# Kernel optimization log

Measured on AMD Instinct MI355X. Metric: run time of the kernel, lower is better.

The kernel has to match this reference:

```python
import jax, jax.numpy as jnp
import numpy as np

THRESHOLD = 0.05
TOP_N = 300
NMS_THR = 0.6
POST_TOP_N = 100
MIN_SIZE = 0
N_CLASS = 81
C = N_CLASS - 1
STRIDES = (8, 16, 32, 64, 128)
IMG_H, IMG_W = 800, 1024
B = 16


def _level_hw(s):
    return (-(-IMG_H // s), -(-IMG_W // s))


def setup_inputs() -> dict:
    key = jax.random.key(0)
    inp = {}
    for li, s in enumerate(STRIDES):
        H, W = _level_hw(s)
        key, k1, k2, k3 = jax.random.split(key, 4)
        xs = (jnp.arange(W, dtype=jnp.float32) + 0.5) * s
        ys = (jnp.arange(H, dtype=jnp.float32) + 0.5) * s
        gx, gy = jnp.meshgrid(xs, ys)  # [H, W], row-major h*W+w flatten order
        inp[f"location{li}"] = jnp.stack([gx.reshape(-1), gy.reshape(-1)], -1)
        inp[f"cls{li}"] = jax.random.normal(k1, (B, C, H, W), jnp.float32)
        inp[f"box{li}"] = jax.random.uniform(k2, (B, 4, H, W), jnp.float32) * (4.0 * s)
        inp[f"ctr{li}"] = jax.random.normal(k3, (B, 1, H, W), jnp.float32)
    inp["img_h"] = IMG_H
    inp["img_w"] = IMG_W
    return inp


def _process_level(loc, cls, box, ctr, img_h, img_w):
    b, c, h, w = cls.shape
    cls = jax.nn.sigmoid(cls.transpose(0, 2, 3, 1).reshape(b, h * w, c))
    box = box.transpose(0, 2, 3, 1).reshape(b, h * w, 4)
    ctr = jax.nn.sigmoid(ctr.reshape(b, h * w))
    score = cls * ctr[:, :, None]                 # [B, HW, C]
    masked = jnp.where(cls > THRESHOLD, score, -1.0).reshape(b, -1)
    k = min(TOP_N, masked.shape[1])
    vals, idx = jax.lax.top_k(masked, k)
    if k < TOP_N:
        vals = jnp.pad(vals, ((0, 0), (0, TOP_N - k)), constant_values=-1.0)
        idx = jnp.pad(idx, ((0, 0), (0, TOP_N - k)))
    valid = vals > 0.0                            # candidates only; pads invalid
    pos = idx // c
    label = idx % c + 1
    ssel = jnp.take_along_axis(score.reshape(b, -1), idx, axis=1)  # differentiable gather
    bsel = jnp.take_along_axis(box, pos[..., None], axis=1)        # [B, TOP_N, 4]
    lsel = loc[pos]                                                # [B, TOP_N, 2]
    # decode + clip (BoxList.clip clamps to [0, size-1])
    x1 = jnp.clip(lsel[..., 0] - bsel[..., 0], 0.0, img_w - 1.0)
    y1 = jnp.clip(lsel[..., 1] - bsel[..., 1], 0.0, img_h - 1.0)
    x2 = jnp.clip(lsel[..., 0] + bsel[..., 2], 0.0, img_w - 1.0)
    y2 = jnp.clip(lsel[..., 1] + bsel[..., 3], 0.0, img_h - 1.0)
    det = jnp.stack([x1, y1, x2, y2], -1)
    # remove_small_box: xywh with remove=1
    valid = valid & ((x2 - x1 + 1.0) >= MIN_SIZE) & ((y2 - y1 + 1.0) >= MIN_SIZE)
    scores = jnp.sqrt(jnp.maximum(ssel, 1e-12))
    return det, scores, label, valid


def _pairwise_iou(b):
    area = (b[:, 2] - b[:, 0]) * (b[:, 3] - b[:, 1])
    lt = jnp.maximum(b[:, None, :2], b[None, :, :2])
    rb = jnp.minimum(b[:, None, 2:], b[None, :, 2:])
    wh = jnp.clip(rb - lt, 0.0)
    inter = wh[..., 0] * wh[..., 1]
    union = area[:, None] + area[None, :] - inter
    return inter / jnp.maximum(union, 1e-9)


def _nms_image(boxes, scores, labels, valid, offset):
    # per-class NMS via class-offset trick: boxes of different labels never overlap
    K = boxes.shape[0]
    s = jnp.where(valid, scores, -jnp.inf)
    order = jnp.argsort(-s)
    b = boxes[order]
    v = valid[order]
    lab = labels[order]
    so = s[order]
    iou = _pairwise_iou(b + (lab.astype(b.dtype) * offset)[:, None])
    ar = jnp.arange(K)

    def body(i, keep):
        sup = (iou[i] > NMS_THR) & keep[i] & (ar > i)
        return keep & ~sup

    keep = jax.lax.fori_loop(0, K, body, v)
    s2 = jnp.where(keep, so, -jnp.inf)
    _, idx2 = jax.lax.top_k(s2, POST_TOP_N)   # post_top_n selection
    fvalid = jnp.take(keep, idx2)
    fb = jnp.where(fvalid[:, None], b[idx2], 0.0)
    fs = jnp.where(fvalid, so[idx2], 0.0)
    fl = jnp.where(fvalid, lab[idx2], 0)
    return fb, fs, fl, fvalid


def _forward(locs, clss, boxs, ctrs, img_h, img_w):
    dets, scs, labs, vals = [], [], [], []
    for loc, cl, bx, ct in zip(locs, clss, boxs, ctrs):
        d, s, l, v = _process_level(loc, cl, bx, ct, float(img_h), float(img_w))
        dets.append(d); scs.append(s); labs.append(l); vals.append(v)
    det = jnp.concatenate(dets, 1)   # [B, 5*TOP_N, 4]
    sc = jnp.concatenate(scs, 1)
    lab = jnp.concatenate(labs, 1)
    val = jnp.concatenate(vals, 1)
    offset = float(max(img_h, img_w) + 1)
    fb, fs, fl, fv = jax.vmap(lambda b_, s_, l_, v_: _nms_image(b_, s_, l_, v_, offset))(det, sc, lab, val)
    out5 = jnp.concatenate([fb, fs[..., None]], -1)  # [B, POST_TOP_N, 5]
    return out5, fl, fv


def reference(location0, location1, location2, location3, location4,
              cls0, cls1, cls2, cls3, cls4,
              box0, box1, box2, box3, box4,
              ctr0, ctr1, ctr2, ctr3, ctr4,
              img_h, img_w):
    locs = [location0, location1, location2, location3, location4]
    clss = [cls0, cls1, cls2, cls3, cls4]
    boxs = [box0, box1, box2, box3, box4]
    ctrs = [ctr0, ctr1, ctr2, ctr3, ctr4]
    return _forward(locs, clss, boxs, ctrs, img_h, img_w)
```

## Files before the change

### kernel.cpp

```cpp
#include <hip/hip_runtime.h>
#include <math.h>

#define THREADS 256
#define SORTT 1024

constexpr int NLEV  = 5;
constexpr int NB    = 16;
constexpr int NC    = 80;
constexpr int TOPN  = 300;
constexpr int KC    = NLEV * TOPN;
constexpr int KROWS = 1536;
constexpr int WORDS = 24;
constexpr int POSTN = 100;
constexpr int CAP   = 4096;
constexpr int NBINS = 2048;
constexpr int NPAIR = NLEV * NB;

constexpr int HW0 = 12800, HW1 = 3200, HW2 = 800, HW3 = 208, HW4 = 56;
constexpr int CH0 = 63, CH1 = 16, CH2 = 4, CH3 = 2, CH4 = 1;
constexpr int CHUNKS = CH0 + CH1 + CH2 + CH3 + CH4;
constexpr int CHUNK_ELEMS = 16384;

constexpr int SCTB0 = 0;
constexpr int SCTB1 = 204800;
constexpr int SCTB2 = 256000;
constexpr int SCTB3 = 268800;
constexpr int SCTB4 = 272128;
constexpr int SCTN  = 273024;

constexpr int GPL0 = 4000, GPL1 = 1000, GPL2 = 250, GPL3 = 65, GPL4 = 18;
constexpr int GMXB0 = 0;
constexpr int GMXB1 = GMXB0 + NB * GPL0;
constexpr int GMXB2 = GMXB1 + NB * GPL1;
constexpr int GMXB3 = GMXB2 + NB * GPL2;
constexpr int GMXB4 = GMXB3 + NB * GPL3;
constexpr int GMXN  = GMXB4 + NB * GPL4;

constexpr size_t align256(size_t x) { return (x + 255) & ~(size_t)255; }
constexpr size_t OFF_HIST = 0;
constexpr size_t OFF_CNT  = OFF_HIST + (size_t)NPAIR * NBINS * 4;
constexpr size_t OFF_CAND = align256(OFF_CNT + (size_t)NPAIR * 4);
constexpr size_t OFF_CBOX = align256(OFF_CAND + (size_t)NPAIR * CAP * 8);
constexpr size_t OFF_CSC  = align256(OFF_CBOX + (size_t)NB * KC * 4 * 4);
constexpr size_t OFF_CLB  = align256(OFF_CSC  + (size_t)NB * KC * 4);
constexpr size_t OFF_SSC  = align256(OFF_CLB  + (size_t)NB * KC * 4);
constexpr size_t OFF_SLB  = align256(OFF_SSC  + (size_t)NB * KC * 4);
constexpr size_t OFF_SBOX = align256(OFF_SLB  + (size_t)NB * KC * 4);
constexpr size_t OFF_OBOX = align256(OFF_SBOX + (size_t)NB * KC * 4 * 4);
constexpr size_t OFF_M    = align256(OFF_OBOX + (size_t)NB * KC * 4 * 4);
constexpr size_t OFF_SCT  = align256(OFF_M + (size_t)NB * KROWS * WORDS * 8);
constexpr size_t OFF_GMX  = align256(OFF_SCT + (size_t)SCTN * 4);
constexpr size_t OFF_TV   = align256(OFF_GMX + (size_t)GMXN * 2);

struct Cand { float s; int i; };

__device__ __forceinline__ float sigm(float x) { return 1.0f / (1.0f + expf(-x)); }

__device__ __forceinline__ float sigf(float x) {
#if __has_builtin(__builtin_amdgcn_exp2f) && __has_builtin(__builtin_amdgcn_rcpf)
    float e = __builtin_amdgcn_exp2f(__fmul_rn(x, -1.44269504088896340736f));
    return __builtin_amdgcn_rcpf(__fadd_rn(1.0f, e));
#else
    return 1.0f / (1.0f + __expf(-x));
#endif
}

__device__ __forceinline__ unsigned scoreKey(float s) {
    unsigned b = __float_as_uint(s);
    unsigned k = (b < 0x3E800000u) ? 0u : ((b - 0x3E800000u) >> 13);
    return (k > 2047u) ? 2047u : k;
}

__device__ __forceinline__ unsigned long long readlane64(unsigned long long v, int l) {
    unsigned lo = (unsigned)__builtin_amdgcn_readlane((int)(unsigned)(v & 0xffffffffull), l);
    unsigned hi = (unsigned)__builtin_amdgcn_readlane((int)(unsigned)(v >> 32), l);
    return ((unsigned long long)hi << 32) | lo;
}

__device__ void bitonicShared(float* ss, int* si, int N) {
    for (int k = 2; k <= N; k <<= 1) {
        for (int j = k >> 1; j > 0; j >>= 1) {
            __syncthreads();
            for (int i = threadIdx.x; i < N; i += blockDim.x) {
                int ixj = i ^ j;
                if (ixj > i) {
                    float s1 = ss[i], s2 = ss[ixj];
                    int a1 = si[i], a2 = si[ixj];
                    bool bef = (s1 > s2) || (s1 == s2 && a1 < a2);
                    bool up = ((i & k) == 0);
                    if (up ? !bef : bef) { ss[i] = s2; ss[ixj] = s1; si[i] = a2; si[ixj] = a1; }
                }
            }
        }
    }
    __syncthreads();
}

__global__ __launch_bounds__(THREADS) void k_init(
        const float* t0, const float* t1, const float* t2, const float* t3, const float* t4,
        float* __restrict__ sct, unsigned* __restrict__ zp, int zn) {
    int i = blockIdx.x * THREADS + threadIdx.x;
    if (i < zn) zp[i] = 0;
    if (i < SCTN) {
        float x;
        if (i < SCTB1)      x = t0[i - SCTB0];
        else if (i < SCTB2) x = t1[i - SCTB1];
        else if (i < SCTB3) x = t2[i - SCTB2];
        else if (i < SCTB4) x = t3[i - SCTB3];
        else                x = t4[i - SCTB4];
        sct[i] = sigm(x);
    }
}

template<int HW, int SCTB, int GPL, int GMXB>
__device__ __forceinline__ void histChunkV(int chunkLocal, int b,
        const float* __restrict__ cls, const float* __restrict__ sct,
        unsigned short* __restrict__ gmx, unsigned* __restrict__ h) {
    constexpr int NE = HW * NC;
    const float* cp = cls + (size_t)b * NE;
    const float* tb = sct + SCTB + b * HW;
    unsigned short* gp = gmx + GMXB + (size_t)b * GPL;
    int w = threadIdx.x >> 6, lane = threadIdx.x & 63;
    int half = lane >> 5, hlane = lane & 31;
    for (int bi = w; bi < 32; bi += 4) {
        int ebase = (chunkLocal * 32 + bi) * 512;
        if (ebase >= NE) break;
        int e = ebase + lane * 8;
        int kmax = 0;
        if (e < NE) {
            int c = e / HW; int hwb = e - c * HW;
            float4 xa = *(const float4*)(cp + e);
            float4 xb = *(const float4*)(cp + e + 4);
            float4 ta = *(const float4*)(tb + hwb);
            float4 tc = *(const float4*)(tb + hwb + 4);
            float xs[8] = {xa.x, xa.y, xa.z, xa.w, xb.x, xb.y, xb.z, xb.w};
            float ts[8] = {ta.x, ta.y, ta.z, ta.w, tc.x, tc.y, tc.z, tc.w};
            #pragma unroll
            for (int q = 0; q < 8; ++q) {
                float scls = sigf(xs[q]);
                float s = __fmul_rn(scls, ts[q]);
                unsigned key = scoreKey(s);
                if (key) atomicAdd(&h[key], 1u);
                kmax = max(kmax, (int)key);
            }
        }
        #pragma unroll
        for (int sh = 1; sh < 32; sh <<= 1) kmax = max(kmax, __shfl_xor(kmax, sh, 64));
        int g = (ebase >> 8) + half;
        if (hlane == 0 && g * 256 < NE) gp[g] = (unsigned short)kmax;
    }
}

__global__ __launch_bounds__(THREADS) void k_hist(
        const float* c0, const float* c1, const float* c2, const float* c3, const float* c4,
        const float* __restrict__ sct, unsigned short* __restrict__ gmx, unsigned* ghist) {
    __shared__ unsigned h[NBINS];
    for (int k = threadIdx.x; k < NBINS; k += THREADS) h[k] = 0;
    __syncthreads();
    int cx = blockIdx.x, b = blockIdx.y;
    int li;
    if (cx < CH0)                 { histChunkV<HW0,SCTB0,GPL0,GMXB0>(cx, b, c0, sct, gmx, h); li = 0; }
    else if (cx < CH0+CH1)        { histChunkV<HW1,SCTB1,GPL1,GMXB1>(cx-CH0, b, c1, sct, gmx, h); li = 1; }
    else if (cx < CH0+CH1+CH2)    { histChunkV<HW2,SCTB2,GPL2,GMXB2>(cx-CH0-CH1, b, c2, sct, gmx, h); li = 2; }
    else if (cx < CH0+CH1+CH2+CH3){ histChunkV<HW3,SCTB3,GPL3,GMXB3>(cx-CH0-CH1-CH2, b, c3, sct, gmx, h); li = 3; }
    else                          { histChunkV<HW4,SCTB4,GPL4,GMXB4>(cx-CH0-CH1-CH2-CH3, b, c4, sct, gmx, h); li = 4; }
    __syncthreads();
    unsigned* gp = ghist + (size_t)(li * NB + b) * NBINS;
    for (int k = threadIdx.x; k < NBINS; k += THREADS) {
        unsigned v = h[k];
        if (v) atomicAdd(&gp[k], v);
    }
}

__global__ __launch_bounds__(THREADS) void k_thresh(
        const unsigned* __restrict__ ghist, unsigned* __restrict__ tvs) {
    __shared__ unsigned seg[THREADS];
    int pid = blockIdx.x;
    const unsigned* h = ghist + (size_t)pid * NBINS;
    constexpr int SB = NBINS / THREADS;
    unsigned s = 0;
    for (int k = 0; k < SB; ++k) s += h[threadIdx.x * SB + k];
    seg[threadIdx.x] = s;
    __syncthreads();
    if (threadIdx.x == 0) {
        unsigned acc = 0; unsigned TA = 0;
        int t = THREADS - 1;
        for (; t >= 0; --t) {
            if (acc + seg[t] >= (unsigned)TOPN) break;
            acc += seg[t];
        }
        if (t >= 0) {
            int lo = t * SB;
            int bin = lo + SB - 1;
            for (; bin >= lo; --bin) { acc += h[bin]; if (acc >= (unsigned)TOPN) break; }
            TA = (unsigned)max(bin, lo);
        }
        tvs[pid] = (TA >= 1) ? (TA - 1) : 0;
    }
}

constexpr int LBUF = 1024;
constexpr int GB = 8;

template<int HW, int SCTB, int GPL, int GMXB>
__device__ __forceinline__ void collectChunkV(int chunkLocal, int b, int li, unsigned Tv,
        const float* __restrict__ cls, const float* __restrict__ sct,
        const unsigned short* __restrict__ gmx,
        Cand* __restrict__ candAll, unsigned* __restrict__ cnt,
        Cand* __restrict__ lbuf, unsigned* __restrict__ lcnt,
        short* __restrict__ glist, int* __restrict__ gcnt) {
    constexpr int NE = HW * NC;
    int pid = li * NB + b;
    Cand* cd = candAll + (size_t)pid * CAP;
    const float* cp = cls + (size_t)b * NE;
    const float* tb = sct + SCTB + b * HW;
    const unsigned short* gp = gmx + GMXB + (size_t)b * GPL;
    if (threadIdx.x < 64) {
        int g = chunkLocal * 64 + threadIdx.x;
        bool ok = ((size_t)g * 256 < (size_t)NE);
        if (ok && Tv) ok = ((unsigned)gp[g] + 1u >= Tv);
        unsigned long long m = __ballot(ok);
        int pos = __popcll(m & ((1ull << threadIdx.x) - 1ull));
        if (ok) glist[pos] = (short)g;
        if (threadIdx.x == 0) *gcnt = __popcll(m);
    }
    __syncthreads();
    int n = *gcnt;
    for (int base = 0; base < n; base += GB) {
        float xv[GB], tv[GB];
        int ev[GB];
        bool okv[GB];
        #pragma unroll
        for (int q = 0; q < GB; ++q) {
            int gi = base + q;
            int g = glist[(gi < n) ? gi : 0];
            int e = g * 256 + (int)threadIdx.x;
            bool ok = (gi < n) && (e < NE);
            e = ok ? e : 0;
            int c = e / HW; int hw = e - c * HW;
            xv[q] = cp[e];
            tv[q] = tb[hw];
            ev[q] = e;
            okv[q] = ok;
        }
        __builtin_amdgcn_sched_barrier(0);
        #pragma unroll
        for (int q = 0; q < GB; ++q) {
            float scls = sigm(xv[q]);
            float s = __fmul_rn(scls, tv[q]);
            unsigned key = scoreKey(s);
            bool take = okv[q] && (Tv ? (key >= Tv) : (scls > 0.05f));
            if (take) {
                int e = ev[q];
                int c = e / HW; int hw = e - c * HW;
                unsigned slot = atomicAdd(lcnt, 1u);
                if (slot < (unsigned)LBUF) { lbuf[slot].s = s; lbuf[slot].i = hw * NC + c; }
                else {
                    unsigned gs = atomicAdd(&cnt[pid], 1u);
                    if (gs < (unsigned)CAP) { cd[gs].s = s; cd[gs].i = hw * NC + c; }
                }
            }
        }
    }
}

__global__ __launch_bounds__(THREADS) void k_collect(
        const float* c0, const float* c1, const float* c2, const float* c3, const float* c4,
        const float* __restrict__ sct, const unsigned short* __restrict__ gmx,
        const unsigned* __restrict__ tvs, Cand* cand, unsigned* cnt) {
    __shared__ Cand lbuf[LBUF];
    __shared__ unsigned lcnt, gbase;
    __shared__ short glist[64];
    __shared__ int gcnt;
    if (threadIdx.x == 0) lcnt = 0;
    int cx = blockIdx.x, b = blockIdx.y;
    int li, cl;
    if (cx < CH0)                  { li = 0; cl = cx; }
    else if (cx < CH0+CH1)         { li = 1; cl = cx - CH0; }
    else if (cx < CH0+CH1+CH2)     { li = 2; cl = cx - CH0 - CH1; }
    else if (cx < CH0+CH1+CH2+CH3) { li = 3; cl = cx - CH0 - CH1 - CH2; }
    else                           { li = 4; cl = cx - CH0 - CH1 - CH2 - CH3; }
    int pid = li * NB + b;
    unsigned Tv = tvs[pid];
    switch (li) {
        case 0: collectChunkV<HW0,SCTB0,GPL0,GMXB0>(cl, b, 0, Tv, c0, sct, gmx, cand, cnt, lbuf, &lcnt, glist, &gcnt); break;
        case 1: collectChunkV<HW1,SCTB1,GPL1,GMXB1>(cl, b, 1, Tv, c1, sct, gmx, cand, cnt, lbuf, &lcnt, glist, &gcnt); break;
        case 2: collectChunkV<HW2,SCTB2,GPL2,GMXB2>(cl, b, 2, Tv, c2, sct, gmx, cand, cnt, lbuf, &lcnt, glist, &gcnt); break;
        case 3: collectChunkV<HW3,SCTB3,GPL3,GMXB3>(cl, b, 3, Tv, c3, sct, gmx, cand, cnt, lbuf, &lcnt, glist, &gcnt); break;
        default: collectChunkV<HW4,SCTB4,GPL4,GMXB4>(cl, b, 4, Tv, c4, sct, gmx, cand, cnt, lbuf, &lcnt, glist, &gcnt); break;
    }
    __syncthreads();
    unsigned n = lcnt; if (n > (unsigned)LBUF) n = LBUF;
    if (threadIdx.x == 0) gbase = n ? atomicAdd(&cnt[pid], n) : 0u;
    __syncthreads();
    Cand* cd = cand + (size_t)pid * CAP;
    for (unsigned i = threadIdx.x; i < n; i += THREADS) {
        unsigned s = gbase + i;
        if (s < (unsigned)CAP) cd[s] = lbuf[i];
    }
}

__global__ __launch_bounds__(THREADS) void k_select(
        const Cand* __restrict__ candAll, const unsigned* __restrict__ cntAll,
        const float* l0, const float* l1, const float* l2, const float* l3, const float* l4,
        const float* b0, const float* b1, const float* b2, const float* b3, const float* b4,
        float* __restrict__ cbox, float* __restrict__ csc, int* __restrict__ clb) {
    __shared__ float ss[CAP];
    __shared__ int si[CAP];
    int pid = blockIdx.x;
    int li = pid / NB, b = pid - li * NB;
    int n = (int)min(cntAll[pid], (unsigned)CAP);
    const Cand* cd = candAll + (size_t)pid * CAP;
    int N = 2; while (N < n) N <<= 1;
    for (int k = threadIdx.x; k < N; k += THREADS) {
        if (k < n) { ss[k] = cd[k].s; si[k] = cd[k].i; }
        else       { ss[k] = -INFINITY; si[k] = 0x40000000 + k; }
    }
    __syncthreads();
    bitonicShared(ss, si, N);

    const float* locp; const float* boxp; int HW;
    switch (li) {
        case 0: locp = l0; boxp = b0; HW = HW0; break;
        case 1: locp = l1; boxp = b1; HW = HW1; break;
        case 2: locp = l2; boxp = b2; HW = HW2; break;
        case 3: locp = l3; boxp = b3; HW = HW3; break;
        default: locp = l4; boxp = b4; HW = HW4; break;
    }
    for (int j = threadIdx.x; j < TOPN; j += THREADS) {
        int cidx = b * KC + li * TOPN + j;
        bool ok = (j < n);
        float s = ok ? ss[j] : -INFINITY;
        ok = ok && (s > 0.0f);
        if (ok) {
            int idx = si[j];
            int hw = idx / NC, c = idx - hw * NC;
            float lx = locp[hw * 2 + 0], ly = locp[hw * 2 + 1];
            const float* bp = boxp + (size_t)b * 4 * HW + hw;
            float bl = bp[0], bt = bp[HW], br = bp[2 * HW], bb = bp[3 * HW];
            float x1 = fminf(fmaxf(__fsub_rn(lx, bl), 0.0f), 1023.0f);
            float y1 = fminf(fmaxf(__fsub_rn(ly, bt), 0.0f),  799.0f);
            float x2 = fminf(fmaxf(__fadd_rn(lx, br), 0.0f), 1023.0f);
            float y2 = fminf(fmaxf(__fadd_rn(ly, bb), 0.0f),  799.0f);
            cbox[cidx * 4 + 0] = x1; cbox[cidx * 4 + 1] = y1;
            cbox[cidx * 4 + 2] = x2; cbox[cidx * 4 + 3] = y2;
            csc[cidx] = sqrtf(fmaxf(s, 1e-12f));
            clb[cidx] = c + 1;
        } else {
            cbox[cidx * 4 + 0] = 0.0f; cbox[cidx * 4 + 1] = 0.0f;
            cbox[cidx * 4 + 2] = 0.0f; cbox[cidx * 4 + 3] = 0.0f;
            csc[cidx] = -INFINITY;
            clb[cidx] = 0;
        }
    }
}

__global__ __launch_bounds__(SORTT) void k_sortimg(
        const float* __restrict__ csc, const int* __restrict__ clb, const float* __restrict__ cbox,
        float* __restrict__ ssc, int* __restrict__ slb, float* __restrict__ sbox, float* __restrict__ obox) {
    int b = blockIdx.x;
    __shared__ float ss[2048];
    __shared__ int si[2048];
    for (int k = threadIdx.x; k < 2048; k += SORTT) {
        if (k < KC) { ss[k] = csc[b * KC + k]; si[k] = k; }
        else        { ss[k] = -INFINITY; si[k] = 0x40000000 + k; }
    }
    __syncthreads();
    bitonicShared(ss, si, 2048);
    for (int k = threadIdx.x; k < KC; k += SORTT) {
        int sl = si[k];
        int src = b * KC + sl;
        int dst = b * KC + k;
        float sc = ss[k];
        int lab = clb[src];
        ssc[dst] = sc; slb[dst] = lab;
        float off = __fmul_rn((float)lab, 1025.0f);
        #pragma unroll
        for (int q = 0; q < 4; ++q) {
            float v = cbox[src * 4 + q];
            sbox[dst * 4 + q] = v;
            obox[dst * 4 + q] = __fadd_rn(v, off);
        }
    }
}

__global__ __launch_bounds__(64) void k_iou(const float* __restrict__ obox,
                                            unsigned long long* __restrict__ MT) {
    int w = blockIdx.x, tile = blockIdx.y, b = blockIdx.z;
    if (w < tile) return;
    int lane = threadIdx.x;
    __shared__ float4 sj[64];
    __shared__ float aj[64];
    const float4* op = (const float4*)obox + (size_t)b * KC;
    int j0 = w * 64;
    int jl = j0 + lane;
    float4 vj = op[(jl < KC) ? jl : (KC - 1)];
    sj[lane] = vj;
    aj[lane] = __fmul_rn(__fsub_rn(vj.z, vj.x), __fsub_rn(vj.w, vj.y));
    int i = tile * 64 + lane;
    float4 bi = op[(i < KC) ? i : (KC - 1)];
    float ai = __fmul_rn(__fsub_rn(bi.z, bi.x), __fsub_rn(bi.w, bi.y));
    __syncthreads();
    unsigned long long bits = 0;
    int jmax = min(64, KC - j0);
    for (int jj = 0; jj < jmax; ++jj) {
        float4 bj = sj[jj];
        float xx1 = fmaxf(bi.x, bj.x), yy1 = fmaxf(bi.y, bj.y);
        float xx2 = fminf(bi.z, bj.z), yy2 = fminf(bi.w, bj.w);
        float ww = fmaxf(__fsub_rn(xx2, xx1), 0.0f);
        float hh = fmaxf(__fsub_rn(yy2, yy1), 0.0f);
        float inter = __fmul_rn(ww, hh);
        float uni = __fsub_rn(__fadd_rn(ai, aj[jj]), inter);
        float iou = __fdiv_rn(inter, fmaxf(uni, 1e-9f));
        bool kp = ((j0 + jj) > i) && (iou > 0.6f);
        bits |= kp ? (1ull << jj) : 0ull;
    }
    if (i >= KC) bits = 0;
    MT[((size_t)b * WORDS + w) * KROWS + i] = bits;
}

__global__ __launch_bounds__(64) void k_nms(
        const unsigned long long* __restrict__ MT, const float* __restrict__ ssc,
        const int* __restrict__ slb, const float* __restrict__ sbox, float* __restrict__ out) {
    int b = blockIdx.x, lane = threadIdx.x;
    for (int k = lane; k < POSTN * 5; k += 64) out[(size_t)b * POSTN * 5 + k] = 0.0f;
    for (int k = lane; k < POSTN; k += 64) {
        out[(size_t)NB * POSTN * 5 + b * POSTN + k] = 0.0f;
        out[(size_t)NB * POSTN * 5 + NB * POSTN + b * POSTN + k] = 0.0f;
    }
    const float* sp = ssc + b * KC;
    unsigned long long validV = 0;
    for (int c = 0; c < WORDS; ++c) {
        int i = c * 64 + lane;
        bool f = (i < KC) && (sp[i] > 0.0f);
        unsigned long long m = __ballot(f);
        validV = (lane == c) ? m : validV;
    }
    unsigned long long mybit = 1ull << lane;
    unsigned long long keptV = 0;
    const unsigned long long* Mb = MT + (size_t)b * WORDS * KROWS;

    unsigned long long pv[WORDS];
    pv[0] = Mb[lane];

    int keptTotal = 0;
    for (int t = 0; t < WORDS; ++t) {
        int tn = (t + 1 < WORDS) ? (t + 1) : t;
        const unsigned long long* cp = Mb + (size_t)tn * KROWS + lane;
        unsigned long long nv[WORDS];
        #pragma unroll
        for (int c = 0; c < WORDS; ++c) {
            int cc = (c <= tn) ? c : 0;
            nv[c] = cp[(size_t)cc * 64];
        }
        __builtin_amdgcn_sched_barrier(0);

        unsigned long long D = pv[t];
        unsigned long long acc = 0;
        #pragma unroll
        for (int c = 0; c < WORDS; ++c) {
            if (c < t) {
                unsigned long long kc = readlane64(keptV, c);
                if (kc & mybit) acc |= pv[c];
            }
        }
        #pragma unroll
        for (int s = 1; s < 64; s <<= 1) acc |= __shfl_xor(acc, s, 64);

        unsigned long long validT = readlane64(validV, t);
        unsigned long long rem = acc;
        unsigned long long sup = __ballot(D != 0ull) & validT;
        unsigned long long todoS = sup;
        while (todoS) {
            int r = __builtin_ctzll(todoS);
            todoS &= todoS - 1;
            if (!((rem >> r) & 1ull)) {
                unsigned long long Dr = readlane64(D, r);
                rem |= Dr;
                todoS &= ~Dr;
            }
        }
        unsigned long long kept = validT & ~rem;
        keptV = (lane == t) ? kept : keptV;

        keptTotal += (int)__popcll(kept);
        if (keptTotal >= POSTN) break;

        #pragma unroll
        for (int c = 0; c < WORDS; ++c) pv[c] = nv[c];
    }

    int base = 0;
    for (int c = 0; c < WORDS && base < POSTN; ++c) {
        unsigned long long kw = readlane64(keptV, c);
        bool f = (kw & mybit) != 0ull;
        int rank = base + __popcll(kw & (mybit - 1ull));
        if (f && rank < POSTN) {
            int i = c * 64 + lane;
            int src = b * KC + i;
            float* o5 = out + ((size_t)b * POSTN + rank) * 5;
            o5[0] = sbox[src * 4 + 0]; o5[1] = sbox[src * 4 + 1];
            o5[2] = sbox[src * 4 + 2]; o5[3] = sbox[src * 4 + 3];
            o5[4] = ssc[src];
            out[(size_t)NB * POSTN * 5 + b * POSTN + rank] = (float)slb[src];
            out[(size_t)NB * POSTN * 5 + NB * POSTN + b * POSTN + rank] = 1.0f;
        }
        base += __popcll(kw);
    }
}

extern "C" void kernel_launch(void* const* d_in, const int* in_sizes, int n_in,
                              void* d_out, int out_size, void* d_ws, size_t ws_size,
                              hipStream_t stream) {
    const float *loc[5], *cls[5], *box[5], *ctr[5];
    for (int l = 0; l < 5; ++l) {
        loc[l] = (const float*)d_in[l * 4 + 0];
        cls[l] = (const float*)d_in[l * 4 + 1];
        box[l] = (const float*)d_in[l * 4 + 2];
        ctr[l] = (const float*)d_in[l * 4 + 3];
    }
    char* ws = (char*)d_ws;
    unsigned* hist = (unsigned*)(ws + OFF_HIST);
    unsigned* cnt  = (unsigned*)(ws + OFF_CNT);
    Cand* cand     = (Cand*)(ws + OFF_CAND);
    float* cbox    = (float*)(ws + OFF_CBOX);
    float* csc     = (float*)(ws + OFF_CSC);
    int*   clb     = (int*)(ws + OFF_CLB);
    float* ssc     = (float*)(ws + OFF_SSC);
    int*   slb     = (int*)(ws + OFF_SLB);
    float* sbox    = (float*)(ws + OFF_SBOX);
    float* obox    = (float*)(ws + OFF_OBOX);
    unsigned long long* MT = (unsigned long long*)(ws + OFF_M);
    float* sct     = (float*)(ws + OFF_SCT);
    unsigned short* gmx = (unsigned short*)(ws + OFF_GMX);
    unsigned* tvs  = (unsigned*)(ws + OFF_TV);
    float* out = (float*)d_out;

    int zn = (int)(OFF_CAND / 4);
    int initBlocks = (max(zn, SCTN) + THREADS - 1) / THREADS;
    k_init<<<initBlocks, THREADS, 0, stream>>>(
        ctr[0], ctr[1], ctr[2], ctr[3], ctr[4], sct, (unsigned*)ws, zn);
    k_hist<<<dim3(CHUNKS, NB), THREADS, 0, stream>>>(
        cls[0], cls[1], cls[2], cls[3], cls[4], sct, gmx, hist);
    k_thresh<<<NPAIR, THREADS, 0, stream>>>(hist, tvs);
    k_collect<<<dim3(CHUNKS, NB), THREADS, 0, stream>>>(
        cls[0], cls[1], cls[2], cls[3], cls[4], sct, gmx, tvs, cand, cnt);
    k_select<<<NPAIR, THREADS, 0, stream>>>(
        cand, cnt,
        loc[0], loc[1], loc[2], loc[3], loc[4],
        box[0], box[1], box[2], box[3], box[4],
        cbox, csc, clb);
    k_sortimg<<<NB, SORTT, 0, stream>>>(csc, clb, cbox, ssc, slb, sbox, obox);
    k_iou<<<dim3(WORDS, WORDS, NB), 64, 0, stream>>>(obox, MT);
    k_nms<<<NB, 64, 0, stream>>>(MT, ssc, slb, sbox, out);
}
```

Before: 290.6 us.

## Compact surviving groups globally in threshold kernel and balance collect work

The threshold kernel now also scans each level/image pair's group-max table and writes a compacted global list of groups that can pass the threshold, plus its count. The collect kernel launches a fixed 16 blocks per pair and splits that compacted list evenly among them, instead of one block per fixed 64-group chunk. This is meant to balance load so blocks that find few surviving groups do not sit idle while others do all the work. It adds a global list write and read and leaves small levels with mostly empty blocks.

After: 280.6 us. 1.04x faster.

```diff
diff --git a/kernel.cpp b/kernel.cpp
--- a/kernel.cpp
+++ b/kernel.cpp
@@ -19,7 +19,6 @@
 constexpr int HW0 = 12800, HW1 = 3200, HW2 = 800, HW3 = 208, HW4 = 56;
 constexpr int CH0 = 63, CH1 = 16, CH2 = 4, CH3 = 2, CH4 = 1;
 constexpr int CHUNKS = CH0 + CH1 + CH2 + CH3 + CH4;
-constexpr int CHUNK_ELEMS = 16384;
 
 constexpr int SCTB0 = 0;
 constexpr int SCTB1 = 204800;
@@ -35,6 +34,9 @@
 constexpr int GMXB3 = GMXB2 + NB * GPL2;
 constexpr int GMXB4 = GMXB3 + NB * GPL3;
 constexpr int GMXN  = GMXB4 + NB * GPL4;
+
+constexpr int GLSTRIDE = 4096;
+constexpr int BPP = 16;
 
 constexpr size_t align256(size_t x) { return (x + 255) & ~(size_t)255; }
 constexpr size_t OFF_HIST = 0;
@@ -51,6 +53,8 @@
 constexpr size_t OFF_SCT  = align256(OFF_M + (size_t)NB * KROWS * WORDS * 8);
 constexpr size_t OFF_GMX  = align256(OFF_SCT + (size_t)SCTN * 4);
 constexpr size_t OFF_TV   = align256(OFF_GMX + (size_t)GMXN * 2);
+constexpr size_t OFF_GCNT = align256(OFF_TV + (size_t)NPAIR * 4);
+constexpr size_t OFF_GL   = align256(OFF_GCNT + (size_t)NPAIR * 4);
 
 struct Cand { float s; int i; };
 
@@ -173,9 +177,13 @@
 }
 
 __global__ __launch_bounds__(THREADS) void k_thresh(
-        const unsigned* __restrict__ ghist, unsigned* __restrict__ tvs) {
+        const unsigned* __restrict__ ghist, const unsigned short* __restrict__ gmx,
+        unsigned* __restrict__ tvs, unsigned* __restrict__ gcntP,
+        unsigned short* __restrict__ glistP) {
     __shared__ unsigned seg[THREADS];
+    __shared__ unsigned shTv, lofs;
     int pid = blockIdx.x;
+    int li = pid >> 4, b = pid & 15;
     const unsigned* h = ghist + (size_t)pid * NBINS;
     constexpr int SB = NBINS / THREADS;
     unsigned s = 0;
@@ -195,47 +203,65 @@
             for (; bin >= lo; --bin) { acc += h[bin]; if (acc >= (unsigned)TOPN) break; }
             TA = (unsigned)max(bin, lo);
         }
-        tvs[pid] = (TA >= 1) ? (TA - 1) : 0;
-    }
+        unsigned Tv = (TA >= 1) ? (TA - 1) : 0;
+        shTv = Tv;
+        tvs[pid] = Tv;
+        lofs = 0;
+    }
+    __syncthreads();
+    unsigned Tv = shTv;
+    int GPL, GMXB;
+    switch (li) {
+        case 0: GPL = GPL0; GMXB = GMXB0; break;
+        case 1: GPL = GPL1; GMXB = GMXB1; break;
+        case 2: GPL = GPL2; GMXB = GMXB2; break;
+        case 3: GPL = GPL3; GMXB = GMXB3; break;
+        default: GPL = GPL4; GMXB = GMXB4; break;
+    }
+    const unsigned short* gp = gmx + GMXB + (size_t)b * GPL;
+    unsigned short* gl = glistP + (size_t)pid * GLSTRIDE;
+    for (int g0 = 0; g0 < GPL; g0 += THREADS) {
+        int g = g0 + (int)threadIdx.x;
+        bool ok = (g < GPL);
+        if (ok && Tv) ok = ((unsigned)gp[g] + 1u >= Tv);
+        unsigned long long m = __ballot(ok);
+        int nW = __popcll(m);
+        if (nW) {
+            unsigned wb = 0;
+            if ((threadIdx.x & 63) == 0) wb = atomicAdd(&lofs, (unsigned)nW);
+            wb = (unsigned)__builtin_amdgcn_readfirstlane((int)wb);
+            if (ok) {
+                unsigned slot = wb + (unsigned)__popcll(m & ((1ull << (threadIdx.x & 63)) - 1ull));
+                gl[slot] = (unsigned short)g;
+            }
+        }
+    }
+    __syncthreads();
+    if (threadIdx.x == 0) gcntP[pid] = lofs;
 }
 
 constexpr int LBUF = 1024;
 constexpr int GB = 8;
 
-template<int HW, int SCTB, int GPL, int GMXB>
-__device__ __forceinline__ void collectChunkV(int chunkLocal, int b, int li, unsigned Tv,
+template<int HW, int SCTB>
+__device__ __forceinline__ void collectRange(int b, int pid, unsigned Tv,
+        unsigned lo, unsigned hi, const unsigned short* __restrict__ gl,
         const float* __restrict__ cls, const float* __restrict__ sct,
-        const unsigned short* __restrict__ gmx,
-        Cand* __restrict__ candAll, unsigned* __restrict__ cnt,
-        Cand* __restrict__ lbuf, unsigned* __restrict__ lcnt,
-        short* __restrict__ glist, int* __restrict__ gcnt) {
+        Cand* __restrict__ cd, unsigned* __restrict__ cnt,
+        Cand* __restrict__ lbuf, unsigned* __restrict__ lcnt) {
     constexpr int NE = HW * NC;
-    int pid = li * NB + b;
-    Cand* cd = candAll + (size_t)pid * CAP;
     const float* cp = cls + (size_t)b * NE;
     const float* tb = sct + SCTB + b * HW;
-    const unsigned short* gp = gmx + GMXB + (size_t)b * GPL;
-    if (threadIdx.x < 64) {
-        int g = chunkLocal * 64 + threadIdx.x;
-        bool ok = ((size_t)g * 256 < (size_t)NE);
-        if (ok && Tv) ok = ((unsigned)gp[g] + 1u >= Tv);
-        unsigned long long m = __ballot(ok);
-        int pos = __popcll(m & ((1ull << threadIdx.x) - 1ull));
-        if (ok) glist[pos] = (short)g;
-        if (threadIdx.x == 0) *gcnt = __popcll(m);
-    }
-    __syncthreads();
-    int n = *gcnt;
-    for (int base = 0; base < n; base += GB) {
+    for (unsigned base = lo; base < hi; base += GB) {
         float xv[GB], tv[GB];
         int ev[GB];
         bool okv[GB];
         #pragma unroll
         for (int q = 0; q < GB; ++q) {
-            int gi = base + q;
-            int g = glist[(gi < n) ? gi : 0];
+            unsigned gi = base + q;
+            int g = gl[(gi < hi) ? gi : (hi - 1)];
             int e = g * 256 + (int)threadIdx.x;
-            bool ok = (gi < n) && (e < NE);
+            bool ok = (gi < hi) && (e < NE);
             e = ok ? e : 0;
             int c = e / HW; int hw = e - c * HW;
             xv[q] = cp[e];
@@ -266,35 +292,36 @@
 
 __global__ __launch_bounds__(THREADS) void k_collect(
         const float* c0, const float* c1, const float* c2, const float* c3, const float* c4,
-        const float* __restrict__ sct, const unsigned short* __restrict__ gmx,
-        const unsigned* __restrict__ tvs, Cand* cand, unsigned* cnt) {
+        const float* __restrict__ sct, const unsigned* __restrict__ tvs,
+        const unsigned* __restrict__ gcntP, const unsigned short* __restrict__ glistP,
+        Cand* cand, unsigned* cnt) {
     __shared__ Cand lbuf[LBUF];
     __shared__ unsigned lcnt, gbase;
-    __shared__ short glist[64];
-    __shared__ int gcnt;
     if (threadIdx.x == 0) lcnt = 0;
-    int cx = blockIdx.x, b = blockIdx.y;
-    int li, cl;
-    if (cx < CH0)                  { li = 0; cl = cx; }
-    else if (cx < CH0+CH1)         { li = 1; cl = cx - CH0; }
-    else if (cx < CH0+CH1+CH2)     { li = 2; cl = cx - CH0 - CH1; }
-    else if (cx < CH0+CH1+CH2+CH3) { li = 3; cl = cx - CH0 - CH1 - CH2; }
-    else                           { li = 4; cl = cx - CH0 - CH1 - CH2 - CH3; }
-    int pid = li * NB + b;
+    __syncthreads();
+    int pid = blockIdx.y;
+    int li = pid >> 4, b = pid & 15;
     unsigned Tv = tvs[pid];
-    switch (li) {
-        case 0: collectChunkV<HW0,SCTB0,GPL0,GMXB0>(cl, b, 0, Tv, c0, sct, gmx, cand, cnt, lbuf, &lcnt, glist, &gcnt); break;
-        case 1: collectChunkV<HW1,SCTB1,GPL1,GMXB1>(cl, b, 1, Tv, c1, sct, gmx, cand, cnt, lbuf, &lcnt, glist, &gcnt); break;
-        case 2: collectChunkV<HW2,SCTB2,GPL2,GMXB2>(cl, b, 2, Tv, c2, sct, gmx, cand, cnt, lbuf, &lcnt, glist, &gcnt); break;
-        case 3: collectChunkV<HW3,SCTB3,GPL3,GMXB3>(cl, b, 3, Tv, c3, sct, gmx, cand, cnt, lbuf, &lcnt, glist, &gcnt); break;
-        default: collectChunkV<HW4,SCTB4,GPL4,GMXB4>(cl, b, 4, Tv, c4, sct, gmx, cand, cnt, lbuf, &lcnt, glist, &gcnt); break;
-    }
-    __syncthreads();
-    unsigned n = lcnt; if (n > (unsigned)LBUF) n = LBUF;
-    if (threadIdx.x == 0) gbase = n ? atomicAdd(&cnt[pid], n) : 0u;
-    __syncthreads();
+    unsigned n = gcntP[pid];
+    unsigned per = (n + BPP - 1) / BPP;
+    unsigned lo = blockIdx.x * per;
+    unsigned hi = min(n, lo + per);
+    const unsigned short* gl = glistP + (size_t)pid * GLSTRIDE;
     Cand* cd = cand + (size_t)pid * CAP;
-    for (unsigned i = threadIdx.x; i < n; i += THREADS) {
+    if (lo < hi) {
+        switch (li) {
+            case 0: collectRange<HW0,SCTB0>(b, pid, Tv, lo, hi, gl, c0, sct, cd, cnt, lbuf, &lcnt); break;
+            case 1: collectRange<HW1,SCTB1>(b, pid, Tv, lo, hi, gl, c1, sct, cd, cnt, lbuf, &lcnt); break;
+            case 2: collectRange<HW2,SCTB2>(b, pid, Tv, lo, hi, gl, c2, sct, cd, cnt, lbuf, &lcnt); break;
+            case 3: collectRange<HW3,SCTB3>(b, pid, Tv, lo, hi, gl, c3, sct, cd, cnt, lbuf, &lcnt); break;
+            default: collectRange<HW4,SCTB4>(b, pid, Tv, lo, hi, gl, c4, sct, cd, cnt, lbuf, &lcnt); break;
+        }
+    }
+    __syncthreads();
+    unsigned nl = lcnt; if (nl > (unsigned)LBUF) nl = LBUF;
+    if (threadIdx.x == 0) gbase = nl ? atomicAdd(&cnt[pid], nl) : 0u;
+    __syncthreads();
+    for (unsigned i = threadIdx.x; i < nl; i += THREADS) {
         unsigned s = gbase + i;
         if (s < (unsigned)CAP) cd[s] = lbuf[i];
     }
@@ -534,6 +561,8 @@
     float* sct     = (float*)(ws + OFF_SCT);
     unsigned short* gmx = (unsigned short*)(ws + OFF_GMX);
     unsigned* tvs  = (unsigned*)(ws + OFF_TV);
+    unsigned* gcntP = (unsigned*)(ws + OFF_GCNT);
+    unsigned short* glistP = (unsigned short*)(ws + OFF_GL);
     float* out = (float*)d_out;
 
     int zn = (int)(OFF_CAND / 4);
@@ -542,9 +571,9 @@
         ctr[0], ctr[1], ctr[2], ctr[3], ctr[4], sct, (unsigned*)ws, zn);
     k_hist<<<dim3(CHUNKS, NB), THREADS, 0, stream>>>(
         cls[0], cls[1], cls[2], cls[3], cls[4], sct, gmx, hist);
-    k_thresh<<<NPAIR, THREADS, 0, stream>>>(hist, tvs);
-    k_collect<<<dim3(CHUNKS, NB), THREADS, 0, stream>>>(
-        cls[0], cls[1], cls[2], cls[3], cls[4], sct, gmx, tvs, cand, cnt);
+    k_thresh<<<NPAIR, THREADS, 0, stream>>>(hist, gmx, tvs, gcntP, glistP);
+    k_collect<<<dim3(BPP, NPAIR), THREADS, 0, stream>>>(
+        cls[0], cls[1], cls[2], cls[3], cls[4], sct, tvs, gcntP, glistP, cand, cnt);
     k_select<<<NPAIR, THREADS, 0, stream>>>(
         cand, cnt,
         loc[0], loc[1], loc[2], loc[3], loc[4],
```
